# Performance work log

Measured on AMD Instinct MI355X. Metric: run time of the kernel, lower is better.

The kernel has to match this reference:

```python
import jax, jax.numpy as jnp
import numpy as np

D_MODEL = 1024
N_HEADS = 16
DH = (D_MODEL // N_HEADS) // 2  # depth // 2 = 32
B, S = 4, 2048


def setup_inputs() -> dict:
    key = jax.random.key(0)
    ks = jax.random.split(key, 8)
    scale_in = 1.0
    q = jax.random.normal(ks[0], (B, S, D_MODEL), dtype=jnp.float32)
    k = jax.random.normal(ks[1], (B, S, D_MODEL), dtype=jnp.float32)
    v = jax.random.normal(ks[2], (B, S, D_MODEL), dtype=jnp.float32)
    # Per-head projection weights stacked over the head axis (glorot-ish init)
    w_std = (2.0 / (D_MODEL + DH)) ** 0.5
    Wq = jax.random.normal(ks[3], (N_HEADS, D_MODEL, DH), dtype=jnp.float32) * w_std
    Wk = jax.random.normal(ks[4], (N_HEADS, D_MODEL, DH), dtype=jnp.float32) * w_std
    Wv = jax.random.normal(ks[5], (N_HEADS, D_MODEL, DH), dtype=jnp.float32) * w_std
    wo_std = (2.0 / (N_HEADS * DH + D_MODEL)) ** 0.5
    Wo = jax.random.normal(ks[6], (N_HEADS * DH, D_MODEL), dtype=jnp.float32) * wo_std
    return {"q": q, "k": k, "v": v, "Wq": Wq, "Wk": Wk, "Wv": Wv, "Wo": Wo}


def reference(q, k, v, Wq, Wk, Wv, Wo):
    # NOTE: source scales by d_model**-0.5 (not head_dim**-0.5)
    scale = D_MODEL ** (-0.5)
    Q = jnp.einsum("bsd,hde->bhse", q, Wq)   # [B,H,S,DH]
    K = jnp.einsum("btd,hde->bhte", k, Wk)
    V = jnp.einsum("btd,hde->bhte", v, Wv)
    attn = jnp.einsum("bhse,bhte->bhst", Q, K) * scale  # [B,H,S,S]
    attn = jax.nn.softmax(attn, axis=-1)
    x = jnp.einsum("bhst,bhte->bhse", attn, V)  # [B,H,S,DH]
    # concat heads along feature dim (head order = concat order in source)
    x = jnp.transpose(x, (0, 2, 1, 3)).reshape(q.shape[0], q.shape[1], N_HEADS * DH)
    return x @ Wo  # [B,S,D_MODEL]; dropout is identity (training=False)
```

## Files before the change

### kernel.cpp

```cpp
#include <hip/hip_runtime.h>
#include <hip/hip_bf16.h>

typedef __attribute__((ext_vector_type(8))) short short8;
typedef __attribute__((ext_vector_type(4))) float f32x4;
typedef __attribute__((ext_vector_type(4))) float fv4;
typedef __attribute__((ext_vector_type(4))) unsigned int u32x4;

#define MFMA16(a, b, c) __builtin_amdgcn_mfma_f32_16x16x32_bf16((a), (b), (c), 0, 0, 0)

typedef const __attribute__((address_space(1))) unsigned int gu32;
typedef __attribute__((address_space(3))) unsigned int lu32;

__device__ __forceinline__ short f2b(float f) {
  unsigned int x = __builtin_bit_cast(unsigned int, f);
  x += 0x7fffu + ((x >> 16) & 1u);
  return (short)(x >> 16);
}

__device__ __forceinline__ unsigned int cvtpk(float lo, float hi) {
  unsigned int r;
  asm("v_cvt_pk_bf16_f32 %0, %1, %2" : "=v"(r) : "v"(lo), "v"(hi));
  return r;
}

#define hexp2(x) __builtin_amdgcn_exp2f(x)

__global__ void prep_weights(const float* __restrict__ Wq, const float* __restrict__ Wk,
                             const float* __restrict__ Wv, const float* __restrict__ Wo,
                             short* __restrict__ WqT, short* __restrict__ WkT,
                             short* __restrict__ WvT, short* __restrict__ WoT) {
  const float SC2 = 0.045084220027780106f;
  int idx = blockIdx.x * 256 + threadIdx.x;
  if (idx < 3 * 512 * 1024) {
    int wsel = idx >> 19;
    int rem = idx & ((1 << 19) - 1);
    int n = rem >> 10;
    int d = rem & 1023;
    const float* W = (wsel == 0) ? Wq : ((wsel == 1) ? Wk : Wv);
    short* WT = (wsel == 0) ? WqT : ((wsel == 1) ? WkT : WvT);
    float v = W[(n >> 5) * (1024 * 32) + d * 32 + (n & 31)];
    if (wsel == 0) v *= SC2;
    WT[n * 1024 + d] = f2b(v);
  } else {
    int idx2 = idx - 3 * 512 * 1024;
    int n = idx2 >> 9;
    int kk = idx2 & 511;
    WoT[n * 512 + kk] = f2b(Wo[kk * 1024 + n]);
  }
}

__global__ __launch_bounds__(512, 2) void proj_gemm(
    const float* __restrict__ q, const float* __restrict__ k, const float* __restrict__ v,
    const short* __restrict__ BTall,
    short* __restrict__ Qb, short* __restrict__ Kb, short* __restrict__ Vtb) {
  __shared__ char smem[98304];
  const int tid = threadIdx.x;
  const int lane = tid & 63;
  const int w = tid >> 6;
  const int l15 = lane & 15, g = lane >> 4;
  const int wm = (w >> 2) * 128;
  const int wn = (w & 3) * 64;
  const int id = blockIdx.x;
  const int mblk = id & 31;
  const int nblk = id >> 5;
  const int zz = nblk >> 1;
  const int bnz = nblk & 1;
  const float* Az = (zz == 0) ? q : ((zz == 1) ? k : v);
  const short* BT = BTall + (size_t)zz * 512 * 1024;
  const int bm0 = mblk * 256;
  const int bn0 = bnz * 256;

  const int ar = lane >> 4;
  const int as_ = lane & 15;
  const int br_ = lane >> 3;
  const int bs_ = lane & 7;

  f32x4 zf = {0.f, 0.f, 0.f, 0.f};
  f32x4 acc[8][4];
#pragma unroll
  for (int a = 0; a < 8; ++a)
#pragma unroll
    for (int bq = 0; bq < 4; ++bq) acc[a][bq] = zf;

  for (int k0 = 0; k0 < 1024; k0 += 64) {
#pragma unroll
    for (int c = 0; c < 8; ++c) {
      int row = 32 * w + 4 * c + ar;
      int s = (as_ & 8) | ((as_ & 7) ^ (row & 7));
      __builtin_amdgcn_global_load_lds(
          (gu32*)(Az + (size_t)(bm0 + row) * 1024 + k0 + 4 * s),
          (lu32*)(smem + w * 8192 + c * 1024), 16, 0, 0);
    }
#pragma unroll
    for (int c = 0; c < 4; ++c) {
      int row = 32 * w + 8 * c + br_;
      int s = bs_ ^ (row & 7);
      __builtin_amdgcn_global_load_lds(
          (gu32*)(BT + (size_t)(bn0 + row) * 1024 + k0 + 8 * s),
          (lu32*)(smem + 65536 + w * 4096 + c * 1024), 16, 0, 0);
    }
    __syncthreads();

#pragma unroll
    for (int kk = 0; kk < 2; ++kk) {
      short8 bfr[4];
#pragma unroll
      for (int nf = 0; nf < 4; ++nf) {
        int row = wn + nf * 16 + l15;
        int s = (4 * kk + g) ^ (row & 7);
        bfr[nf] = *(const short8*)(smem + 65536 + row * 128 + s * 16);
      }
#pragma unroll
      for (int mf = 0; mf < 8; ++mf) {
        int row = wm + mf * 16 + l15;
        int s0 = 8 * kk + 2 * g;
        int sa = (s0 & 8) | ((s0 & 7) ^ (row & 7));
        int sb = ((s0 + 1) & 8) | (((s0 + 1) & 7) ^ (row & 7));
        fv4 a0 = *(const fv4*)(smem + row * 256 + sa * 16);
        fv4 a1 = *(const fv4*)(smem + row * 256 + sb * 16);
        u32x4 wv;
        wv[0] = cvtpk(a0[0], a0[1]);
        wv[1] = cvtpk(a0[2], a0[3]);
        wv[2] = cvtpk(a1[0], a1[1]);
        wv[3] = cvtpk(a1[2], a1[3]);
        short8 af = __builtin_bit_cast(short8, wv);
#pragma unroll
        for (int nf = 0; nf < 4; ++nf)
          acc[mf][nf] = MFMA16(af, bfr[nf], acc[mf][nf]);
      }
    }
    __syncthreads();
  }

#pragma unroll
  for (int mf = 0; mf < 8; ++mf)
#pragma unroll
    for (int nf = 0; nf < 4; ++nf)
#pragma unroll
      for (int i = 0; i < 4; ++i) {
        int row = bm0 + wm + mf * 16 + g * 4 + i;
        int col = bn0 + wn + nf * 16 + l15;
        int bb = row >> 11, ss = row & 2047;
        int hh = col >> 5, ee = col & 31;
        short val = f2b(acc[mf][nf][i]);
        if (zz == 2)
          Vtb[((size_t)(bb * 16 + hh) * 32 + ee) * 2048 + ss] = val;
        else if (zz == 1)
          Kb[((size_t)(bb * 16 + hh) * 2048 + ss) * 32 + ee] = val;
        else
          Qb[((size_t)(bb * 16 + hh) * 2048 + ss) * 32 + ee] = val;
      }
}

__global__ __launch_bounds__(256, 2) void out_gemm(const short* __restrict__ X,
                                                   const short* __restrict__ WoT,
                                                   float* __restrict__ out) {
  __shared__ char smem[32768];
  const int tid = threadIdx.x;
  const int lane = tid & 63;
  const int w = tid >> 6;
  const int l15 = lane & 15, g = lane >> 4;
  const int wm = (w >> 1) * 64, wn = (w & 1) * 64;
  const int id = blockIdx.x;
  const int bm0 = (id & 63) * 128, bn0 = (id >> 6) * 128;

  const int br = (lane >> 2);
  const int bu = lane & 3;

  f32x4 zf = {0.f, 0.f, 0.f, 0.f};
  f32x4 acc[4][4];
#pragma unroll
  for (int a = 0; a < 4; ++a)
#pragma unroll
    for (int bq = 0; bq < 4; ++bq) acc[a][bq] = zf;

#define STAGE(base, k0)                                                        \
  {                                                                            \
    _Pragma("unroll") for (int i = 0; i < 2; ++i) {                            \
      int row = 32 * w + 16 * i + br;                                          \
      __builtin_amdgcn_global_load_lds(                                        \
          (gu32*)(X + (size_t)(bm0 + row) * 512 + (k0) +                       \
                  8 * (bu ^ ((row >> 1) & 3))),                                \
          (lu32*)(smem + (base) + w * 2048 + i * 1024), 16, 0, 0);             \
      __builtin_amdgcn_global_load_lds(                                        \
          (gu32*)(WoT + (size_t)(bn0 + row) * 512 + (k0) +                     \
                  8 * (bu ^ ((row >> 1) & 3))),                                \
          (lu32*)(smem + (base) + 8192 + w * 2048 + i * 1024), 16, 0, 0);      \
    }                                                                          \
  }

#define COMPUTE(base)                                                          \
  {                                                                            \
    short8 af[4], bfr[4];                                                      \
    _Pragma("unroll") for (int mf = 0; mf < 4; ++mf) {                         \
      int row = wm + mf * 16 + l15;                                            \
      af[mf] = *(const short8*)(smem + (base) + row * 64 +                     \
                                ((g ^ ((row >> 1) & 3)) * 16));                \
    }                                                                          \
    _Pragma("unroll") for (int nf = 0; nf < 4; ++nf) {                         \
      int row = wn + nf * 16 + l15;                                            \
      bfr[nf] = *(const short8*)(smem + (base) + 8192 + row * 64 +             \
                                 ((g ^ ((row >> 1) & 3)) * 16));               \
    }                                                                          \
    _Pragma("unroll") for (int mf = 0; mf < 4; ++mf)                           \
        _Pragma("unroll") for (int nf = 0; nf < 4; ++nf)                       \
            acc[mf][nf] = MFMA16(af[mf], bfr[nf], acc[mf][nf]);                \
  }

  STAGE(0, 0);
  for (int k0 = 0; k0 < 512; k0 += 32) {
    const int cur = (k0 >> 5) & 1;
    const int cbase = cur * 16384;
    const int nbase = (cur ^ 1) * 16384;
    if (k0 + 32 < 512) {
      STAGE(nbase, k0 + 32);
      asm volatile("s_waitcnt vmcnt(4)" ::: "memory");
    } else {
      asm volatile("s_waitcnt vmcnt(0)" ::: "memory");
    }
    __builtin_amdgcn_s_barrier();
    COMPUTE(cbase);
    __builtin_amdgcn_s_barrier();
  }
#undef STAGE
#undef COMPUTE

#pragma unroll
  for (int mf = 0; mf < 4; ++mf)
#pragma unroll
    for (int nf = 0; nf < 4; ++nf)
#pragma unroll
      for (int i = 0; i < 4; ++i) {
        int row = bm0 + wm + mf * 16 + g * 4 + i;
        int col = bn0 + wn + nf * 16 + l15;
        out[(size_t)row * 1024 + col] = acc[mf][nf][i];
      }
}

__device__ __forceinline__ void qk_half(short8 k0, short8 k1, short8 k2, short8 k3,
                                        short8 qf, const f32x4& zf,
                                        short8& pf0, short8& pf1) {
  f32x4 s0 = MFMA16(k0, qf, zf);
  f32x4 s1 = MFMA16(k1, qf, zf);
  f32x4 s2 = MFMA16(k2, qf, zf);
  f32x4 s3 = MFMA16(k3, qf, zf);
#pragma unroll
  for (int i = 0; i < 4; ++i) {
    s0[i] = hexp2(s0[i]);
    s1[i] = hexp2(s1[i]);
    s2[i] = hexp2(s2[i]);
    s3[i] = hexp2(s3[i]);
  }
  u32x4 w0, w1;
  w0[0] = cvtpk(s0[0], s0[1]);
  w0[1] = cvtpk(s0[2], s0[3]);
  w0[2] = cvtpk(s1[0], s1[1]);
  w0[3] = cvtpk(s1[2], s1[3]);
  w1[0] = cvtpk(s2[0], s2[1]);
  w1[1] = cvtpk(s2[2], s2[3]);
  w1[2] = cvtpk(s3[0], s3[1]);
  w1[3] = cvtpk(s3[2], s3[3]);
  pf0 = __builtin_bit_cast(short8, w0);
  pf1 = __builtin_bit_cast(short8, w1);
}

__global__ __launch_bounds__(256, 4) void attn(const short* __restrict__ Qb,
                                               const short* __restrict__ Kb,
                                               const short* __restrict__ Vtb,
                                               short* __restrict__ X) {
  __shared__ short KV[2][2][2048];
  const int tid = threadIdx.x;
  const int lane = tid & 63;
  const int w = tid >> 6;
  const int l15 = lane & 15, g = lane >> 4;
  const int id = blockIdx.x;
  const int bh = id & 63;
  const int qblk = id >> 6;
  const int bb = bh >> 4, hh = bh & 15;
  const int q0 = qblk * 128 + w * 32;

  const short* Qp = Qb + ((size_t)bh * 2048 + q0) * 32;
  const short* Kp = Kb + (size_t)bh * 2048 * 32;
  const short* Vp = Vtb + (size_t)bh * 32 * 2048;

  short8 qfA = *(const short8*)(Qp + l15 * 32 + g * 8);
  short8 qfB = *(const short8*)(Qp + (16 + l15) * 32 + g * 8);

  const int kbase = 8 * (l15 >> 2) + (l15 & 3);
  const int koff = (w & 1) * 4 + (w >> 1) * 32;
  const int vrow = (w >> 1) * 16;
  const int vcol = (w & 1) * 32;
  const short* Ksrc0 = Kp + (size_t)(kbase + koff) * 32 + g * 8;
  const short* Vsrc0 = Vp + (size_t)(l15 + vrow) * 2048 + vcol + g * 8;

  f32x4 zf = {0.f, 0.f, 0.f, 0.f};
  f32x4 o_loA = zf, o_hiA = zf, o_loB = zf, o_hiB = zf;
  f32x4 accLA = zf, accLB = zf;
  u32x4 ones_u = {0x3F803F80u, 0x3F803F80u, 0x3F803F80u, 0x3F803F80u};
  const short8 ones = __builtin_bit_cast(short8, ones_u);

#define STAGE(b, t0)                                                        \
  {                                                                         \
    __builtin_amdgcn_global_load_lds((gu32*)(Ksrc0 + (size_t)(t0) * 32),    \
                                     (lu32*)&KV[b][0][w * 512], 16, 0, 0);  \
    __builtin_amdgcn_global_load_lds((gu32*)(Vsrc0 + (t0)),                 \
                                     (lu32*)&KV[b][1][w * 512], 16, 0, 0);  \
  }

#define BODY(b)                                                       \
  {                                                                   \
    short8 k0 = *(const short8*)(&KV[b][0][0 * 512 + lane * 8]);      \
    short8 k1 = *(const short8*)(&KV[b][0][1 * 512 + lane * 8]);      \
    short8 k2 = *(const short8*)(&KV[b][0][2 * 512 + lane * 8]);      \
    short8 k3 = *(const short8*)(&KV[b][0][3 * 512 + lane * 8]);      \
    short8 vlo0 = *(const short8*)(&KV[b][1][0 * 512 + lane * 8]);    \
    short8 vlo1 = *(const short8*)(&KV[b][1][1 * 512 + lane * 8]);    \
    short8 vhi0 = *(const short8*)(&KV[b][1][2 * 512 + lane * 8]);    \
    short8 vhi1 = *(const short8*)(&KV[b][1][3 * 512 + lane * 8]);    \
    short8 pfA0, pfA1, pfB0, pfB1;                                    \
    qk_half(k0, k1, k2, k3, qfA, zf, pfA0, pfA1);                     \
    qk_half(k0, k1, k2, k3, qfB, zf, pfB0, pfB1);                     \
    __builtin_amdgcn_s_setprio(1);                                    \
    accLA = MFMA16(pfA0, ones, accLA);                                \
    accLA = MFMA16(pfA1, ones, accLA);                                \
    accLB = MFMA16(pfB0, ones, accLB);                                \
    accLB = MFMA16(pfB1, ones, accLB);                                \
    o_loA = MFMA16(pfA0, vlo0, o_loA);                                \
    o_loA = MFMA16(pfA1, vlo1, o_loA);                                \
    o_hiA = MFMA16(pfA0, vhi0, o_hiA);                                \
    o_hiA = MFMA16(pfA1, vhi1, o_hiA);                                \
    o_loB = MFMA16(pfB0, vlo0, o_loB);                                \
    o_loB = MFMA16(pfB1, vlo1, o_loB);                                \
    o_hiB = MFMA16(pfB0, vhi0, o_hiB);                                \
    o_hiB = MFMA16(pfB1, vhi1, o_hiB);                                \
    __builtin_amdgcn_s_setprio(0);                                    \
  }

  STAGE(0, 0);
  __syncthreads();
  for (int t0 = 0; t0 < 2048; t0 += 128) {
    STAGE(1, t0 + 64);
    BODY(0);
    __syncthreads();
    if (t0 + 128 < 2048) {
      STAGE(0, t0 + 128);
    }
    BODY(1);
    __syncthreads();
  }
#undef STAGE
#undef BODY

#pragma unroll
  for (int i = 0; i < 4; ++i) {
    float invA = 1.0f / accLA[i];
    float invB = 1.0f / accLB[i];
    int ssA = q0 + 4 * g + i;
    size_t baseA = ((size_t)bb * 2048 + ssA) * 512 + hh * 32;
    X[baseA + l15] = f2b(o_loA[i] * invA);
    X[baseA + 16 + l15] = f2b(o_hiA[i] * invA);
    size_t baseB = baseA + (size_t)16 * 512;
    X[baseB + l15] = f2b(o_loB[i] * invB);
    X[baseB + 16 + l15] = f2b(o_hiB[i] * invB);
  }
}

extern "C" void kernel_launch(void* const* d_in, const int* in_sizes, int n_in,
                              void* d_out, int out_size, void* d_ws, size_t ws_size,
                              hipStream_t stream) {
  const float* q = (const float*)d_in[0];
  const float* k = (const float*)d_in[1];
  const float* v = (const float*)d_in[2];
  const float* Wq = (const float*)d_in[3];
  const float* Wk = (const float*)d_in[4];
  const float* Wv = (const float*)d_in[5];
  const float* Wo = (const float*)d_in[6];

  char* ws = (char*)d_ws;
  const size_t MB = 1u << 20;
  short* WqT = (short*)(ws + 0 * MB);
  short* WkT = (short*)(ws + 1 * MB);
  short* WvT = (short*)(ws + 2 * MB);
  short* WoT = (short*)(ws + 3 * MB);
  short* Qb  = (short*)(ws + 4 * MB);
  short* Kb  = (short*)(ws + 12 * MB);
  short* Vtb = (short*)(ws + 20 * MB);
  short* Xb  = (short*)(ws + 28 * MB);

  prep_weights<<<8192, 256, 0, stream>>>(Wq, Wk, Wv, Wo, WqT, WkT, WvT, WoT);
  proj_gemm<<<192, 512, 0, stream>>>(q, k, v, WqT, Qb, Kb, Vtb);
  attn<<<1024, 256, 0, stream>>>(Qb, Kb, Vtb, Xb);
  out_gemm<<<512, 256, 0, stream>>>(Xb, WoT, (float*)d_out);
}
```

Measured before the change: 143.2 us.

## Shrink projection GEMM tiles to 128x128 with smaller blocks and raise MFMA priority

The projection GEMM moves from 256x256 tiles with 512-thread blocks and 96KB of LDS to 128x128 tiles with 256-thread blocks, a K step of 32, and 24KB of LDS. The grid grows from 192 to 768 blocks, which fills the 256 CUs and allows more resident blocks per CU. Both GEMMs now raise wave priority around the MFMA bursts with s_setprio, and out_gemm gets a sched_barrier after its barrier. The cost is lower data reuse per tile and more global traffic, since the fp32 activations are reloaded for more N-tiles.

```diff
diff --git a/kernel.cpp b/kernel.cpp
--- a/kernel.cpp
+++ b/kernel.cpp
@@ -7,6 +7,8 @@
 typedef __attribute__((ext_vector_type(4))) unsigned int u32x4;
 
 #define MFMA16(a, b, c) __builtin_amdgcn_mfma_f32_16x16x32_bf16((a), (b), (c), 0, 0, 0)
+#define SBAR() __builtin_amdgcn_sched_barrier(0)
+#define RBAR() __builtin_amdgcn_s_barrier()
 
 typedef const __attribute__((address_space(1))) unsigned int gu32;
 typedef __attribute__((address_space(3))) unsigned int lu32;
@@ -49,97 +51,94 @@
   }
 }
 
-__global__ __launch_bounds__(512, 2) void proj_gemm(
+__global__ __launch_bounds__(256, 4) void proj_gemm(
     const float* __restrict__ q, const float* __restrict__ k, const float* __restrict__ v,
     const short* __restrict__ BTall,
     short* __restrict__ Qb, short* __restrict__ Kb, short* __restrict__ Vtb) {
-  __shared__ char smem[98304];
+  __shared__ char smem[24576];
   const int tid = threadIdx.x;
   const int lane = tid & 63;
   const int w = tid >> 6;
   const int l15 = lane & 15, g = lane >> 4;
-  const int wm = (w >> 2) * 128;
-  const int wn = (w & 3) * 64;
+  const int wm = (w >> 1) * 64, wn = (w & 1) * 64;
   const int id = blockIdx.x;
-  const int mblk = id & 31;
-  const int nblk = id >> 5;
-  const int zz = nblk >> 1;
-  const int bnz = nblk & 1;
+  const int bm = id & 63;
+  const int bn = id >> 6;
+  const int zz = bn >> 2;
+  const int bnz = bn & 3;
   const float* Az = (zz == 0) ? q : ((zz == 1) ? k : v);
   const short* BT = BTall + (size_t)zz * 512 * 1024;
-  const int bm0 = mblk * 256;
-  const int bn0 = bnz * 256;
-
-  const int ar = lane >> 4;
-  const int as_ = lane & 15;
-  const int br_ = lane >> 3;
-  const int bs_ = lane & 7;
+  const int bm0 = bm * 128, bn0z = bnz * 128;
+
+  const int ar = lane >> 3;
+  const int au = lane & 7;
+  const int br = lane >> 2;
+  const int bu = lane & 3;
 
   f32x4 zf = {0.f, 0.f, 0.f, 0.f};
-  f32x4 acc[8][4];
-#pragma unroll
-  for (int a = 0; a < 8; ++a)
+  f32x4 acc[4][4];
+#pragma unroll
+  for (int a = 0; a < 4; ++a)
 #pragma unroll
     for (int bq = 0; bq < 4; ++bq) acc[a][bq] = zf;
 
-  for (int k0 = 0; k0 < 1024; k0 += 64) {
-#pragma unroll
-    for (int c = 0; c < 8; ++c) {
-      int row = 32 * w + 4 * c + ar;
-      int s = (as_ & 8) | ((as_ & 7) ^ (row & 7));
+  for (int k0 = 0; k0 < 1024; k0 += 32) {
+#pragma unroll
+    for (int i = 0; i < 4; ++i) {
+      int rowa = 32 * w + 8 * i + ar;
       __builtin_amdgcn_global_load_lds(
-          (gu32*)(Az + (size_t)(bm0 + row) * 1024 + k0 + 4 * s),
-          (lu32*)(smem + w * 8192 + c * 1024), 16, 0, 0);
-    }
-#pragma unroll
-    for (int c = 0; c < 4; ++c) {
-      int row = 32 * w + 8 * c + br_;
-      int s = bs_ ^ (row & 7);
+          (gu32*)(Az + (size_t)(bm0 + rowa) * 1024 + k0 + 4 * (au ^ (rowa & 7))),
+          (lu32*)(smem + w * 4096 + i * 1024), 16, 0, 0);
+    }
+#pragma unroll
+    for (int i = 0; i < 2; ++i) {
+      int rowb = 32 * w + 16 * i + br;
       __builtin_amdgcn_global_load_lds(
-          (gu32*)(BT + (size_t)(bn0 + row) * 1024 + k0 + 8 * s),
-          (lu32*)(smem + 65536 + w * 4096 + c * 1024), 16, 0, 0);
+          (gu32*)(BT + (size_t)(bn0z + rowb) * 1024 + k0 +
+                  8 * (bu ^ ((rowb >> 1) & 3))),
+          (lu32*)(smem + 16384 + w * 2048 + i * 1024), 16, 0, 0);
     }
     __syncthreads();
 
-#pragma unroll
-    for (int kk = 0; kk < 2; ++kk) {
-      short8 bfr[4];
+    {
+      short8 af[4], bfr[4];
 #pragma unroll
       for (int nf = 0; nf < 4; ++nf) {
         int row = wn + nf * 16 + l15;
-        int s = (4 * kk + g) ^ (row & 7);
-        bfr[nf] = *(const short8*)(smem + 65536 + row * 128 + s * 16);
+        bfr[nf] = *(const short8*)(smem + 16384 + row * 64 +
+                                   ((g ^ ((row >> 1) & 3)) * 16));
       }
 #pragma unroll
-      for (int mf = 0; mf < 8; ++mf) {
+      for (int mf = 0; mf < 4; ++mf) {
         int row = wm + mf * 16 + l15;
-        int s0 = 8 * kk + 2 * g;
-        int sa = (s0 & 8) | ((s0 & 7) ^ (row & 7));
-        int sb = ((s0 + 1) & 8) | (((s0 + 1) & 7) ^ (row & 7));
-        fv4 a0 = *(const fv4*)(smem + row * 256 + sa * 16);
-        fv4 a1 = *(const fv4*)(smem + row * 256 + sb * 16);
+        fv4 a0 = *(const fv4*)(smem + row * 128 + (((2 * g) ^ (row & 7)) * 16));
+        fv4 a1 = *(const fv4*)(smem + row * 128 + (((2 * g + 1) ^ (row & 7)) * 16));
         u32x4 wv;
         wv[0] = cvtpk(a0[0], a0[1]);
         wv[1] = cvtpk(a0[2], a0[3]);
         wv[2] = cvtpk(a1[0], a1[1]);
         wv[3] = cvtpk(a1[2], a1[3]);
-        short8 af = __builtin_bit_cast(short8, wv);
+        af[mf] = __builtin_bit_cast(short8, wv);
+      }
+      __builtin_amdgcn_s_setprio(1);
+#pragma unroll
+      for (int mf = 0; mf < 4; ++mf)
 #pragma unroll
         for (int nf = 0; nf < 4; ++nf)
-          acc[mf][nf] = MFMA16(af, bfr[nf], acc[mf][nf]);
-      }
+          acc[mf][nf] = MFMA16(af[mf], bfr[nf], acc[mf][nf]);
+      __builtin_amdgcn_s_setprio(0);
     }
     __syncthreads();
   }
 
 #pragma unroll
-  for (int mf = 0; mf < 8; ++mf)
+  for (int mf = 0; mf < 4; ++mf)
 #pragma unroll
     for (int nf = 0; nf < 4; ++nf)
 #pragma unroll
       for (int i = 0; i < 4; ++i) {
         int row = bm0 + wm + mf * 16 + g * 4 + i;
-        int col = bn0 + wn + nf * 16 + l15;
+        int col = bn0z + wn + nf * 16 + l15;
         int bb = row >> 11, ss = row & 2047;
         int hh = col >> 5, ee = col & 31;
         short val = f2b(acc[mf][nf][i]);
@@ -202,9 +201,11 @@
       bfr[nf] = *(const short8*)(smem + (base) + 8192 + row * 64 +             \
                                  ((g ^ ((row >> 1) & 3)) * 16));               \
     }                                                                          \
+    __builtin_amdgcn_s_setprio(1);                                             \
     _Pragma("unroll") for (int mf = 0; mf < 4; ++mf)                           \
         _Pragma("unroll") for (int nf = 0; nf < 4; ++nf)                       \
             acc[mf][nf] = MFMA16(af[mf], bfr[nf], acc[mf][nf]);                \
+    __builtin_amdgcn_s_setprio(0);                                             \
   }
 
   STAGE(0, 0);
@@ -218,9 +219,10 @@
     } else {
       asm volatile("s_waitcnt vmcnt(0)" ::: "memory");
     }
-    __builtin_amdgcn_s_barrier();
+    RBAR();
+    SBAR();
     COMPUTE(cbase);
-    __builtin_amdgcn_s_barrier();
+    RBAR();
   }
 #undef STAGE
 #undef COMPUTE
@@ -388,7 +390,7 @@
   short* Xb  = (short*)(ws + 28 * MB);
 
   prep_weights<<<8192, 256, 0, stream>>>(Wq, Wk, Wv, Wo, WqT, WkT, WvT, WoT);
-  proj_gemm<<<192, 512, 0, stream>>>(q, k, v, WqT, Qb, Kb, Vtb);
+  proj_gemm<<<768, 256, 0, stream>>>(q, k, v, WqT, Qb, Kb, Vtb);
   attn<<<1024, 256, 0, stream>>>(Qb, Kb, Vtb, Xb);
   out_gemm<<<512, 256, 0, stream>>>(Xb, WoT, (float*)d_out);
 }
```

Result: faster. 119.3 us (-16.6%).
